# Optimization experiments

Measured on AMD Instinct MI355X. Metric: run time of the kernel, lower is better.

Reference implementation:

```python
import jax, jax.numpy as jnp
import numpy as np

DIM = 384
HEADS = 12
HEAD_DIM = DIM // HEADS
WS = 7


def setup_inputs() -> dict:
    key = jax.random.key(0)
    k0, k1, k2, k3, k4 = jax.random.split(key, 5)
    x = jax.random.normal(k0, (16, DIM, 56, 56), dtype=jnp.float32)
    s = 1.0 / np.sqrt(DIM)
    Wqkv = jax.random.normal(k1, (DIM, 3 * DIM), dtype=jnp.float32) * s
    bqkv = jax.random.normal(k2, (3 * DIM,), dtype=jnp.float32) * 0.01
    Wproj = jax.random.normal(k3, (DIM, DIM), dtype=jnp.float32) * s
    bproj = jax.random.normal(k4, (DIM,), dtype=jnp.float32) * 0.01
    return {"x": x, "Wqkv": Wqkv, "bqkv": bqkv, "Wproj": Wproj, "bproj": bproj}


def _window_attention(x, Wqkv, bqkv, Wproj, bproj):
    B, D, H, W = x.shape
    x = jnp.transpose(x, (0, 2, 3, 1))  # (B, H, W, D)
    pad_h = (WS - H % WS) % WS
    pad_w = (WS - W % WS) % WS
    if pad_h or pad_w:
        x = jnp.pad(x, ((0, 0), (0, pad_h), (0, pad_w), (0, 0)))
    Hp, Wp = x.shape[1], x.shape[2]
    nH, nW = Hp // WS, Wp // WS
    # window partition: (B*nH*nW, WS*WS, D)
    xw = x.reshape(B, nH, WS, nW, WS, D).transpose(0, 1, 3, 2, 4, 5)
    windows = xw.reshape(B * nH * nW, WS * WS, D)
    BnW, N, _ = windows.shape
    qkv = windows @ Wqkv + bqkv  # (BnW, N, 3D)
    qkv = qkv.reshape(BnW, N, 3, HEADS, HEAD_DIM).transpose(2, 0, 3, 1, 4)
    q, k, v = qkv[0], qkv[1], qkv[2]  # (BnW, heads, N, hd)
    scale = HEAD_DIM ** -0.5
    attn = jnp.einsum('bhnd,bhmd->bhnm', q, k) * scale
    attn = jax.nn.softmax(attn, axis=-1)
    out = jnp.einsum('bhnm,bhmd->bhnd', attn, v)  # (BnW, heads, N, hd)
    out = out.transpose(0, 2, 1, 3).reshape(BnW, N, D)
    out = out @ Wproj + bproj
    # window reverse
    x = out.reshape(B, nH, nW, WS, WS, D).transpose(0, 1, 3, 2, 4, 5)
    x = x.reshape(B, Hp, Wp, D)
    if pad_h or pad_w:
        x = x[:, :H, :W, :]
    return jnp.transpose(x, (0, 3, 1, 2))  # (B, D, H, W)


def reference(x, Wqkv, bqkv, Wproj, bproj):
    return _window_attention(x, Wqkv, bqkv, Wproj, bproj)
```

## Files before the change

### kernel.cpp

```cpp
#include <hip/hip_runtime.h>

#define TOK     50176
#define NQKV    1152
#define DMODEL  384
#define HW      3136
#define NWIN    1024

typedef __bf16 bf16x8 __attribute__((ext_vector_type(8)));
typedef float  f32x4  __attribute__((ext_vector_type(4)));

__device__ __forceinline__ __bf16 f2bf(float f) {
  unsigned u = __float_as_uint(f);
  u += 0x7fffu + ((u >> 16) & 1u);
  unsigned short s = (unsigned short)(u >> 16);
  return __builtin_bit_cast(__bf16, s);
}
__device__ __forceinline__ unsigned short f2bfu(float f) {
  return __builtin_bit_cast(unsigned short, f2bf(f));
}
__device__ __forceinline__ float bf2f(__bf16 b) {
  return __uint_as_float(((unsigned)__builtin_bit_cast(unsigned short, b)) << 16);
}
__device__ __forceinline__ void gload_lds16(const void* g, void* l) {
  __builtin_amdgcn_global_load_lds(
      (const __attribute__((address_space(1))) unsigned int*)g,
      (__attribute__((address_space(3))) unsigned int*)l, 16, 0, 0);
}

__global__ __launch_bounds__(256) void gather_x(const float* __restrict__ x,
                                                __bf16* __restrict__ Xw) {
  __shared__ __bf16 lt[392 * 48];
  const int ct = blockIdx.x, hr = blockIdx.y, b = blockIdx.z;
  const int tid = threadIdx.x;
  const float* xb = x + ((size_t)(b * 384 + ct * 48)) * HW + hr * 7 * 56;

  for (int u = tid; u < 48 * 7 * 14; u += 256) {
    const int ch = u / 98, rem = u % 98;
    const int h7 = rem / 14, w4 = rem % 14;
    const float4 v = *(const float4*)&xb[(size_t)ch * HW + h7 * 56 + 4 * w4];
    const float vv[4] = {v.x, v.y, v.z, v.w};
#pragma unroll
    for (int e = 0; e < 4; ++e) {
      const int w = 4 * w4 + e;
      const int t = (w / 7) * 49 + h7 * 7 + (w % 7);
      lt[t * 48 + ch] = f2bf(vv[e]);
    }
  }
  __syncthreads();

  const size_t tokbase = (size_t)(b * 64 + hr * 8) * 49;
  for (int u = tid; u < 392 * 6; u += 256) {
    const int t = u / 6, c6 = u % 6;
    const bf16x8 vv = *(const bf16x8*)&lt[t * 48 + 8 * c6];
    *(bf16x8*)&Xw[(tokbase + t) * DMODEL + ct * 48 + 8 * c6] = vv;
  }
}

__global__ __launch_bounds__(256) void unscatter(const __bf16* __restrict__ P,
                                                 float* __restrict__ out) {
  __shared__ __bf16 lt[392 * 48];
  const int ct = blockIdx.x, hr = blockIdx.y, b = blockIdx.z;
  const int tid = threadIdx.x;
  const size_t tokbase = (size_t)(b * 64 + hr * 8) * 49;

  for (int u = tid; u < 392 * 6; u += 256) {
    const int t = u / 6, c6 = u % 6;
    *(bf16x8*)&lt[t * 48 + 8 * c6] =
        *(const bf16x8*)&P[(tokbase + t) * DMODEL + ct * 48 + 8 * c6];
  }
  __syncthreads();

  float* ob = out + ((size_t)(b * 384 + ct * 48)) * HW + hr * 7 * 56;
  for (int u = tid; u < 48 * 98; u += 256) {
    const int ch = u / 98, rem = u % 98;
    const int h7 = rem / 14, w4 = rem % 14;
    float4 o;
    float* oo = (float*)&o;
#pragma unroll
    for (int e = 0; e < 4; ++e) {
      const int w = 4 * w4 + e;
      const int t = (w / 7) * 49 + h7 * 7 + (w % 7);
      oo[e] = bf2f(lt[t * 48 + ch]);
    }
    *(float4*)&ob[(size_t)ch * HW + h7 * 56 + 4 * w4] = o;
  }
}

__global__ void conv_w(const float* __restrict__ Wqkv, const float* __restrict__ Wproj,
                       __bf16* __restrict__ WqkvT, __bf16* __restrict__ WprojT) {
  const int idx = blockIdx.x * 256 + threadIdx.x;
  if (idx < DMODEL * NQKV) {
    const int k = idx / NQKV, n = idx % NQKV;
    WqkvT[(size_t)n * DMODEL + k] = f2bf(Wqkv[idx]);
  }
  if (idx < DMODEL * DMODEL) {
    const int k = idx / DMODEL, n = idx % DMODEL;
    WprojT[(size_t)n * DMODEL + k] = f2bf(Wproj[idx]);
  }
}

__global__ __launch_bounds__(512) void gemm256(const __bf16* __restrict__ A,
                                               const __bf16* __restrict__ BT,
                                               const float* __restrict__ bias,
                                               __bf16* __restrict__ Cout, int Ncols) {
  __shared__ __align__(16) __bf16 As[3][256 * 32];
  __shared__ __align__(16) __bf16 Bs[3][128 * 32];
  const int tid  = threadIdx.x;
  const int lane = tid & 63;
  const int wid  = tid >> 6;

  const int nwg  = gridDim.x * gridDim.y;
  const int orig = blockIdx.y * gridDim.x + blockIdx.x;
  const int q    = nwg >> 3, r = nwg & 7;
  const int xcd  = orig & 7, pos = orig >> 3;
  const int start = (xcd < r) ? xcd * (q + 1) : r * (q + 1) + (xcd - r) * q;
  const int w    = start + pos;
  const int bn   = (w % gridDim.x) << 7;
  const int bm   = (w / gridDim.x) << 8;

  const __bf16* a0 = A  + (size_t)(bm +       (tid >> 2)) * DMODEL + ((tid & 3) << 3);
  const __bf16* a1 = A  + (size_t)(bm + 128 + (tid >> 2)) * DMODEL + ((tid & 3) << 3);
  const __bf16* b0 = BT + (size_t)(bn +       (tid >> 2)) * DMODEL + ((tid & 3) << 3);

  const int wm = (wid >> 1) << 6;
  const int wn = (wid & 1) << 6;
  const int lrow = lane & 15;
  const int lk8  = (lane >> 4) << 3;

  f32x4 acc[4][4] = {};

  auto stage = [&](int buf, int kt) {
    const int koff = kt << 5;
    gload_lds16(a0 + koff, &As[buf][(wid << 9)]);
    gload_lds16(a1 + koff, &As[buf][4096 + (wid << 9)]);
    gload_lds16(b0 + koff, &Bs[buf][(wid << 9)]);
  };

  stage(0, 0);
  stage(1, 1);
#pragma unroll 1
  for (int kt = 0; kt < 12; ++kt) {
    asm volatile("s_waitcnt vmcnt(3)" ::: "memory");
    __builtin_amdgcn_sched_barrier(0);
    __builtin_amdgcn_s_barrier();
    __builtin_amdgcn_sched_barrier(0);
    asm volatile("" ::: "memory");

    const int nt = (kt + 2 < 12) ? (kt + 2) : (kt - 10);
    stage((kt + 2) % 3, nt);

    const int buf = kt % 3;
    const __bf16* pA = &As[buf][(wm + lrow) * 32 + lk8];
    const __bf16* pB = &Bs[buf][(wn + lrow) * 32 + lk8];
    bf16x8 av[4], bv[4];
#pragma unroll
    for (int i = 0; i < 4; ++i) av[i] = *(const bf16x8*)(pA + i * 16 * 32);
#pragma unroll
    for (int j = 0; j < 4; ++j) bv[j] = *(const bf16x8*)(pB + j * 16 * 32);
#pragma unroll
    for (int i = 0; i < 4; ++i)
#pragma unroll
      for (int j = 0; j < 4; ++j)
        acc[j][i] = __builtin_amdgcn_mfma_f32_16x16x32_bf16(bv[j], av[i], acc[j][i], 0, 0, 0);
  }

  const int lr = lane & 15, g = lane >> 4;
  const int tok0 = bm + wm + lr;
  const int ch0  = bn + wn + (g << 2);

#pragma unroll
  for (int j = 0; j < 4; ++j) {
    const int ch = ch0 + 16 * j;
    const float4 b4 = *(const float4*)&bias[ch];
#pragma unroll
    for (int i = 0; i < 4; ++i) {
      const int token = tok0 + 16 * i;
      ushort4 pk;
      pk.x = f2bfu(acc[j][i][0] + b4.x);
      pk.y = f2bfu(acc[j][i][1] + b4.y);
      pk.z = f2bfu(acc[j][i][2] + b4.z);
      pk.w = f2bfu(acc[j][i][3] + b4.w);
      *(ushort4*)&Cout[(size_t)token * Ncols + ch] = pk;
    }
  }
}

__global__ __launch_bounds__(64) void attn_mfma(const __bf16* __restrict__ qkv,
                                                __bf16* __restrict__ attnO) {
  __shared__ __align__(16) __bf16 lds[96 * 72];
  __bf16* p_lds = lds;
  __bf16* vt    = lds + 64 * 72;

  const int lane = threadIdx.x;
  const int win  = blockIdx.x;
  const int h    = blockIdx.y;
  const int lr = lane & 15, g = lane >> 4;
  const size_t rowbase = (size_t)win * 49;

  int rr[4];
#pragma unroll
  for (int f = 0; f < 4; ++f) rr[f] = (16 * f + lr > 48) ? 48 : (16 * f + lr);

  const int co = h * 32 + 8 * g;

  bf16x8 av[4], bv[4];
#pragma unroll
  for (int f = 0; f < 4; ++f) {
    const __bf16* rp = qkv + (rowbase + rr[f]) * NQKV + co;
    av[f] = *(const bf16x8*)(rp + 384);
    bv[f] = *(const bf16x8*)(rp);
  }

  ushort4 vreg[7];
#pragma unroll
  for (int u = 0; u < 7; ++u) {
    const int unit = lane + (u << 6);
    if (unit < 392) {
      const int k = unit >> 3, dq = unit & 7;
      vreg[u] = *(const ushort4*)(qkv + (rowbase + k) * NQKV + 768 + h * 32 + 4 * dq);
    }
  }

  f32x4 acc[4][4] = {};
#pragma unroll
  for (int i = 0; i < 4; ++i)
#pragma unroll
    for (int j = 0; j < 4; ++j)
      acc[i][j] = __builtin_amdgcn_mfma_f32_16x16x32_bf16(av[i], bv[j], acc[i][j], 0, 0, 0);

  const float scale = 0.17677669529663687f;
#pragma unroll
  for (int i = 0; i < 4; ++i)
#pragma unroll
    for (int j = 0; j < 4; ++j)
#pragma unroll
      for (int r = 0; r < 4; ++r) {
        float v = acc[i][j][r] * scale;
        if (i == 3 && (4 * g + r) != 0) v = -1e30f;
        acc[i][j][r] = v;
      }

#pragma unroll
  for (int u = 0; u < 7; ++u) {
    const int unit = lane + (u << 6);
    if (unit < 392) {
      const int k = unit >> 3, dq = unit & 7;
      const ushort4 vv = vreg[u];
      vt[(4 * dq + 0) * 72 + k] = __builtin_bit_cast(__bf16, vv.x);
      vt[(4 * dq + 1) * 72 + k] = __builtin_bit_cast(__bf16, vv.y);
      vt[(4 * dq + 2) * 72 + k] = __builtin_bit_cast(__bf16, vv.z);
      vt[(4 * dq + 3) * 72 + k] = __builtin_bit_cast(__bf16, vv.w);
    }
  }

#pragma unroll
  for (int j = 0; j < 4; ++j) {
    float mx = -1e30f;
#pragma unroll
    for (int i = 0; i < 4; ++i)
#pragma unroll
      for (int r = 0; r < 4; ++r) mx = fmaxf(mx, acc[i][j][r]);
    mx = fmaxf(mx, __shfl_xor(mx, 16));
    mx = fmaxf(mx, __shfl_xor(mx, 32));
    float sum = 0.f;
#pragma unroll
    for (int i = 0; i < 4; ++i)
#pragma unroll
      for (int r = 0; r < 4; ++r) {
        const float e = __expf(acc[i][j][r] - mx);
        acc[i][j][r] = e;
        sum += e;
      }
    sum += __shfl_xor(sum, 16);
    sum += __shfl_xor(sum, 32);
    const float inv = 1.f / sum;
#pragma unroll
    for (int i = 0; i < 4; ++i) {
      ushort4 pk;
      pk.x = f2bfu(acc[i][j][0] * inv);
      pk.y = f2bfu(acc[i][j][1] * inv);
      pk.z = f2bfu(acc[i][j][2] * inv);
      pk.w = f2bfu(acc[i][j][3] * inv);
      *(ushort4*)&p_lds[(16 * j + lr) * 72 + 16 * i + 4 * g] = pk;
    }
  }

  f32x4 o[2][4] = {};
#pragma unroll
  for (int ks = 0; ks < 2; ++ks) {
    bf16x8 a2[2], b2[4];
#pragma unroll
    for (int i2 = 0; i2 < 2; ++i2)
      a2[i2] = *(const bf16x8*)&vt[(16 * i2 + lr) * 72 + 32 * ks + 8 * g];
#pragma unroll
    for (int j2 = 0; j2 < 4; ++j2)
      b2[j2] = *(const bf16x8*)&p_lds[(16 * j2 + lr) * 72 + 32 * ks + 8 * g];
#pragma unroll
    for (int i2 = 0; i2 < 2; ++i2)
#pragma unroll
      for (int j2 = 0; j2 < 4; ++j2)
        o[i2][j2] = __builtin_amdgcn_mfma_f32_16x16x32_bf16(a2[i2], b2[j2], o[i2][j2], 0, 0, 0);
  }

#pragma unroll
  for (int j2 = 0; j2 < 4; ++j2) {
    const int q = 16 * j2 + lr;
    if (q <= 48) {
#pragma unroll
      for (int i2 = 0; i2 < 2; ++i2) {
        ushort4 ok;
        ok.x = f2bfu(o[i2][j2][0]);
        ok.y = f2bfu(o[i2][j2][1]);
        ok.z = f2bfu(o[i2][j2][2]);
        ok.w = f2bfu(o[i2][j2][3]);
        *(ushort4*)&attnO[(rowbase + q) * DMODEL + h * 32 + 16 * i2 + 4 * g] = ok;
      }
    }
  }
}

extern "C" void kernel_launch(void* const* d_in, const int* in_sizes, int n_in,
                              void* d_out, int out_size, void* d_ws, size_t ws_size,
                              hipStream_t stream) {
  const float* x     = (const float*)d_in[0];
  const float* Wqkv  = (const float*)d_in[1];
  const float* bqkv  = (const float*)d_in[2];
  const float* Wproj = (const float*)d_in[3];
  const float* bproj = (const float*)d_in[4];
  float* out = (float*)d_out;

  char* ws = (char*)d_ws;
  __bf16* Xw     = (__bf16*)ws;  ws += (size_t)TOK * DMODEL * 2;
  __bf16* qkvb   = (__bf16*)ws;  ws += (size_t)TOK * NQKV * 2;
  __bf16* attnO  = (__bf16*)ws;  ws += (size_t)TOK * DMODEL * 2;
  __bf16* attnP  = (__bf16*)ws;  ws += (size_t)TOK * DMODEL * 2;
  __bf16* WqkvT  = (__bf16*)ws;  ws += (size_t)NQKV * DMODEL * 2;
  __bf16* WprojT = (__bf16*)ws;

  gather_x<<<dim3(8, 8, 16), 256, 0, stream>>>(x, Xw);
  conv_w<<<1728, 256, 0, stream>>>(Wqkv, Wproj, WqkvT, WprojT);
  gemm256<<<dim3(NQKV / 128, TOK / 256), 512, 0, stream>>>(Xw, WqkvT, bqkv, qkvb, NQKV);
  attn_mfma<<<dim3(NWIN, 12), 64, 0, stream>>>(qkvb, attnO);
  gemm256<<<dim3(DMODEL / 128, TOK / 256), 512, 0, stream>>>(attnO, WprojT, bproj, attnP, DMODEL);
  unscatter<<<dim3(8, 8, 16), 256, 0, stream>>>(attnP, out);
}
```

Before: 229.4 us.

## Split QKV GEMM k-step into two halves with interleaved loads and setprio

Restructures the triple-buffered main loop of the QKV GEMM. Global-to-LDS prefetches for the next stage are now issued between two halves of the MFMA work: A tiles before the first half, B tile after a mid-iteration barrier. MFMA blocks are wrapped in s_setprio raises. The goal is better overlap of memory issue with compute and less scheduler contention, at the cost of an extra workgroup barrier per k-step.

```diff
diff --git a/kernel.cpp b/kernel.cpp
--- a/kernel.cpp
+++ b/kernel.cpp
@@ -129,39 +129,64 @@
 
   f32x4 acc[4][4] = {};
 
-  auto stage = [&](int buf, int kt) {
-    const int koff = kt << 5;
-    gload_lds16(a0 + koff, &As[buf][(wid << 9)]);
-    gload_lds16(a1 + koff, &As[buf][4096 + (wid << 9)]);
-    gload_lds16(b0 + koff, &Bs[buf][(wid << 9)]);
-  };
-
-  stage(0, 0);
-  stage(1, 1);
+  {
+    gload_lds16(a0, &As[0][(wid << 9)]);
+    gload_lds16(a1, &As[0][4096 + (wid << 9)]);
+    gload_lds16(b0, &Bs[0][(wid << 9)]);
+    gload_lds16(a0 + 32, &As[1][(wid << 9)]);
+    gload_lds16(a1 + 32, &As[1][4096 + (wid << 9)]);
+    gload_lds16(b0 + 32, &Bs[1][(wid << 9)]);
+  }
+  asm volatile("s_waitcnt vmcnt(3)" ::: "memory");
+  __builtin_amdgcn_sched_barrier(0);
+  __builtin_amdgcn_s_barrier();
+  __builtin_amdgcn_sched_barrier(0);
+
 #pragma unroll 1
   for (int kt = 0; kt < 12; ++kt) {
-    asm volatile("s_waitcnt vmcnt(3)" ::: "memory");
-    __builtin_amdgcn_sched_barrier(0);
-    __builtin_amdgcn_s_barrier();
-    __builtin_amdgcn_sched_barrier(0);
-    asm volatile("" ::: "memory");
-
-    const int nt = (kt + 2 < 12) ? (kt + 2) : (kt - 10);
-    stage((kt + 2) % 3, nt);
-
     const int buf = kt % 3;
+    const int dst = (kt + 2) % 3;
+    const int nt  = (kt + 2 < 12) ? (kt + 2) : (kt - 10);
+    const int koff = nt << 5;
     const __bf16* pA = &As[buf][(wm + lrow) * 32 + lk8];
     const __bf16* pB = &Bs[buf][(wn + lrow) * 32 + lk8];
-    bf16x8 av[4], bv[4];
-#pragma unroll
-    for (int i = 0; i < 4; ++i) av[i] = *(const bf16x8*)(pA + i * 16 * 32);
+
+    gload_lds16(a0 + koff, &As[dst][(wid << 9)]);
+    gload_lds16(a1 + koff, &As[dst][4096 + (wid << 9)]);
+    bf16x8 bv[4], av0, av1;
 #pragma unroll
     for (int j = 0; j < 4; ++j) bv[j] = *(const bf16x8*)(pB + j * 16 * 32);
-#pragma unroll
-    for (int i = 0; i < 4; ++i)
-#pragma unroll
-      for (int j = 0; j < 4; ++j)
-        acc[j][i] = __builtin_amdgcn_mfma_f32_16x16x32_bf16(bv[j], av[i], acc[j][i], 0, 0, 0);
+    av0 = *(const bf16x8*)(pA);
+    av1 = *(const bf16x8*)(pA + 16 * 32);
+    __builtin_amdgcn_s_setprio(1);
+#pragma unroll
+    for (int j = 0; j < 4; ++j)
+      acc[j][0] = __builtin_amdgcn_mfma_f32_16x16x32_bf16(bv[j], av0, acc[j][0], 0, 0, 0);
+#pragma unroll
+    for (int j = 0; j < 4; ++j)
+      acc[j][1] = __builtin_amdgcn_mfma_f32_16x16x32_bf16(bv[j], av1, acc[j][1], 0, 0, 0);
+    __builtin_amdgcn_s_setprio(0);
+    __builtin_amdgcn_sched_barrier(0);
+    __builtin_amdgcn_s_barrier();
+    __builtin_amdgcn_sched_barrier(0);
+
+    gload_lds16(b0 + koff, &Bs[dst][(wid << 9)]);
+    bf16x8 av2, av3;
+    av2 = *(const bf16x8*)(pA + 2 * 16 * 32);
+    av3 = *(const bf16x8*)(pA + 3 * 16 * 32);
+    __builtin_amdgcn_s_setprio(1);
+#pragma unroll
+    for (int j = 0; j < 4; ++j)
+      acc[j][2] = __builtin_amdgcn_mfma_f32_16x16x32_bf16(bv[j], av2, acc[j][2], 0, 0, 0);
+#pragma unroll
+    for (int j = 0; j < 4; ++j)
+      acc[j][3] = __builtin_amdgcn_mfma_f32_16x16x32_bf16(bv[j], av3, acc[j][3], 0, 0, 0);
+    __builtin_amdgcn_s_setprio(0);
+    __builtin_amdgcn_sched_barrier(0);
+    asm volatile("s_waitcnt vmcnt(3)" ::: "memory");
+    __builtin_amdgcn_sched_barrier(0);
+    __builtin_amdgcn_s_barrier();
+    __builtin_amdgcn_sched_barrier(0);
   }
 
   const int lr = lane & 15, g = lane >> 4;
```

Result: no change. 228.4 us (-0.4%).

## Widen GEMM tile to 256x256 with padded N and restructured prefetch barrier

Applied to the files above, without the earlier changes.

Grows the GEMM block tile from 256x128 to 256x256, so each wave computes 128x64 with more MFMAs per LDS load. To fit the wider tile, the QKV output is padded from 1152 to 1280 columns and the projection output from 384 to 512, with zero-filled weights and biases. The loop now issues the prefetch before the MFMAs, raises wave priority around the MFMA block, and moves the wait and barrier to the end of each iteration. The padding adds wasted work, about 11% for QKV and a third for the projection, and more LDS and registers per block.

```diff
diff --git a/kernel.cpp b/kernel.cpp
--- a/kernel.cpp
+++ b/kernel.cpp
@@ -2,7 +2,9 @@
 
 #define TOK     50176
 #define NQKV    1152
+#define NQKVP   1280
 #define DMODEL  384
+#define PROJP   512
 #define HW      3136
 #define NWIN    1024
 
@@ -66,7 +68,7 @@
   for (int u = tid; u < 392 * 6; u += 256) {
     const int t = u / 6, c6 = u % 6;
     *(bf16x8*)&lt[t * 48 + 8 * c6] =
-        *(const bf16x8*)&P[(tokbase + t) * DMODEL + ct * 48 + 8 * c6];
+        *(const bf16x8*)&P[(tokbase + t) * PROJP + ct * 48 + 8 * c6];
   }
   __syncthreads();
 
@@ -87,16 +89,20 @@
 }
 
 __global__ void conv_w(const float* __restrict__ Wqkv, const float* __restrict__ Wproj,
-                       __bf16* __restrict__ WqkvT, __bf16* __restrict__ WprojT) {
+                       const float* __restrict__ bqkv, const float* __restrict__ bproj,
+                       __bf16* __restrict__ WqkvT, __bf16* __restrict__ WprojT,
+                       float* __restrict__ bqkvP, float* __restrict__ bprojP) {
   const int idx = blockIdx.x * 256 + threadIdx.x;
-  if (idx < DMODEL * NQKV) {
-    const int k = idx / NQKV, n = idx % NQKV;
-    WqkvT[(size_t)n * DMODEL + k] = f2bf(Wqkv[idx]);
-  }
-  if (idx < DMODEL * DMODEL) {
-    const int k = idx / DMODEL, n = idx % DMODEL;
-    WprojT[(size_t)n * DMODEL + k] = f2bf(Wproj[idx]);
-  }
+  if (idx < NQKVP * DMODEL) {
+    const int n = idx / DMODEL, k = idx % DMODEL;
+    WqkvT[idx] = (n < NQKV) ? f2bf(Wqkv[(size_t)k * NQKV + n]) : (__bf16)0.0f;
+  }
+  if (idx < PROJP * DMODEL) {
+    const int n = idx / DMODEL, k = idx % DMODEL;
+    WprojT[idx] = (n < DMODEL) ? f2bf(Wproj[(size_t)k * DMODEL + n]) : (__bf16)0.0f;
+  }
+  if (idx < NQKVP) bqkvP[idx] = (idx < NQKV) ? bqkv[idx] : 0.f;
+  if (idx < PROJP) bprojP[idx] = (idx < DMODEL) ? bproj[idx] : 0.f;
 }
 
 __global__ __launch_bounds__(512) void gemm256(const __bf16* __restrict__ A,
@@ -104,7 +110,7 @@
                                                const float* __restrict__ bias,
                                                __bf16* __restrict__ Cout, int Ncols) {
   __shared__ __align__(16) __bf16 As[3][256 * 32];
-  __shared__ __align__(16) __bf16 Bs[3][128 * 32];
+  __shared__ __align__(16) __bf16 Bs[3][256 * 32];
   const int tid  = threadIdx.x;
   const int lane = tid & 63;
   const int wid  = tid >> 6;
@@ -115,53 +121,62 @@
   const int xcd  = orig & 7, pos = orig >> 3;
   const int start = (xcd < r) ? xcd * (q + 1) : r * (q + 1) + (xcd - r) * q;
   const int w    = start + pos;
-  const int bn   = (w % gridDim.x) << 7;
+  const int bn   = (w % gridDim.x) << 8;
   const int bm   = (w / gridDim.x) << 8;
 
-  const __bf16* a0 = A  + (size_t)(bm +       (tid >> 2)) * DMODEL + ((tid & 3) << 3);
-  const __bf16* a1 = A  + (size_t)(bm + 128 + (tid >> 2)) * DMODEL + ((tid & 3) << 3);
-  const __bf16* b0 = BT + (size_t)(bn +       (tid >> 2)) * DMODEL + ((tid & 3) << 3);
-
-  const int wm = (wid >> 1) << 6;
-  const int wn = (wid & 1) << 6;
+  const __bf16* a0 = A  + (size_t)(bm + (tid >> 2)) * DMODEL + ((tid & 3) << 3);
+  const __bf16* a1 = a0 + (size_t)128 * DMODEL;
+  const __bf16* b0 = BT + (size_t)(bn + (tid >> 2)) * DMODEL + ((tid & 3) << 3);
+  const __bf16* b1 = b0 + (size_t)128 * DMODEL;
+
+  const int wm = (wid >> 2) << 7;
+  const int wn = (wid & 3) << 6;
   const int lrow = lane & 15;
   const int lk8  = (lane >> 4) << 3;
 
-  f32x4 acc[4][4] = {};
+  f32x4 acc[4][8] = {};
 
   auto stage = [&](int buf, int kt) {
     const int koff = kt << 5;
     gload_lds16(a0 + koff, &As[buf][(wid << 9)]);
     gload_lds16(a1 + koff, &As[buf][4096 + (wid << 9)]);
     gload_lds16(b0 + koff, &Bs[buf][(wid << 9)]);
+    gload_lds16(b1 + koff, &Bs[buf][4096 + (wid << 9)]);
   };
 
   stage(0, 0);
   stage(1, 1);
+  asm volatile("s_waitcnt vmcnt(4)" ::: "memory");
+  __builtin_amdgcn_sched_barrier(0);
+  __builtin_amdgcn_s_barrier();
+  __builtin_amdgcn_sched_barrier(0);
+
 #pragma unroll 1
   for (int kt = 0; kt < 12; ++kt) {
-    asm volatile("s_waitcnt vmcnt(3)" ::: "memory");
+    const int buf = kt % 3;
+    const int dst = (kt + 2) % 3;
+    const int nt  = (kt + 2 < 12) ? (kt + 2) : (kt - 10);
+    stage(dst, nt);
+
+    const __bf16* pA = &As[buf][(wm + lrow) * 32 + lk8];
+    const __bf16* pB = &Bs[buf][(wn + lrow) * 32 + lk8];
+    bf16x8 av[8], bv[4];
+#pragma unroll
+    for (int i = 0; i < 8; ++i) av[i] = *(const bf16x8*)(pA + i * 16 * 32);
+#pragma unroll
+    for (int j = 0; j < 4; ++j) bv[j] = *(const bf16x8*)(pB + j * 16 * 32);
+    __builtin_amdgcn_s_setprio(1);
+#pragma unroll
+    for (int i = 0; i < 8; ++i)
+#pragma unroll
+      for (int j = 0; j < 4; ++j)
+        acc[j][i] = __builtin_amdgcn_mfma_f32_16x16x32_bf16(bv[j], av[i], acc[j][i], 0, 0, 0);
+    __builtin_amdgcn_s_setprio(0);
+    __builtin_amdgcn_sched_barrier(0);
+    asm volatile("s_waitcnt vmcnt(4)" ::: "memory");
     __builtin_amdgcn_sched_barrier(0);
     __builtin_amdgcn_s_barrier();
     __builtin_amdgcn_sched_barrier(0);
-    asm volatile("" ::: "memory");
-
-    const int nt = (kt + 2 < 12) ? (kt + 2) : (kt - 10);
-    stage((kt + 2) % 3, nt);
-
-    const int buf = kt % 3;
-    const __bf16* pA = &As[buf][(wm + lrow) * 32 + lk8];
-    const __bf16* pB = &Bs[buf][(wn + lrow) * 32 + lk8];
-    bf16x8 av[4], bv[4];
-#pragma unroll
-    for (int i = 0; i < 4; ++i) av[i] = *(const bf16x8*)(pA + i * 16 * 32);
-#pragma unroll
-    for (int j = 0; j < 4; ++j) bv[j] = *(const bf16x8*)(pB + j * 16 * 32);
-#pragma unroll
-    for (int i = 0; i < 4; ++i)
-#pragma unroll
-      for (int j = 0; j < 4; ++j)
-        acc[j][i] = __builtin_amdgcn_mfma_f32_16x16x32_bf16(bv[j], av[i], acc[j][i], 0, 0, 0);
   }
 
   const int lr = lane & 15, g = lane >> 4;
@@ -173,7 +188,7 @@
     const int ch = ch0 + 16 * j;
     const float4 b4 = *(const float4*)&bias[ch];
 #pragma unroll
-    for (int i = 0; i < 4; ++i) {
+    for (int i = 0; i < 8; ++i) {
       const int token = tok0 + 16 * i;
       ushort4 pk;
       pk.x = f2bfu(acc[j][i][0] + b4.x);
@@ -206,7 +221,7 @@
   bf16x8 av[4], bv[4];
 #pragma unroll
   for (int f = 0; f < 4; ++f) {
-    const __bf16* rp = qkv + (rowbase + rr[f]) * NQKV + co;
+    const __bf16* rp = qkv + (rowbase + rr[f]) * NQKVP + co;
     av[f] = *(const bf16x8*)(rp + 384);
     bv[f] = *(const bf16x8*)(rp);
   }
@@ -217,7 +232,7 @@
     const int unit = lane + (u << 6);
     if (unit < 392) {
       const int k = unit >> 3, dq = unit & 7;
-      vreg[u] = *(const ushort4*)(qkv + (rowbase + k) * NQKV + 768 + h * 32 + 4 * dq);
+      vreg[u] = *(const ushort4*)(qkv + (rowbase + k) * NQKVP + 768 + h * 32 + 4 * dq);
     }
   }
 
@@ -331,16 +346,19 @@
 
   char* ws = (char*)d_ws;
   __bf16* Xw     = (__bf16*)ws;  ws += (size_t)TOK * DMODEL * 2;
-  __bf16* qkvb   = (__bf16*)ws;  ws += (size_t)TOK * NQKV * 2;
+  __bf16* qkvb   = (__bf16*)ws;  ws += (size_t)TOK * NQKVP * 2;
   __bf16* attnO  = (__bf16*)ws;  ws += (size_t)TOK * DMODEL * 2;
-  __bf16* attnP  = (__bf16*)ws;  ws += (size_t)TOK * DMODEL * 2;
-  __bf16* WqkvT  = (__bf16*)ws;  ws += (size_t)NQKV * DMODEL * 2;
-  __bf16* WprojT = (__bf16*)ws;
+  __bf16* attnP  = (__bf16*)ws;  ws += (size_t)TOK * PROJP * 2;
+  __bf16* WqkvT  = (__bf16*)ws;  ws += (size_t)NQKVP * DMODEL * 2;
+  __bf16* WprojT = (__bf16*)ws;  ws += (size_t)PROJP * DMODEL * 2;
+  float*  bqkvP  = (float*)ws;   ws += NQKVP * 4;
+  float*  bprojP = (float*)ws;
 
   gather_x<<<dim3(8, 8, 16), 256, 0, stream>>>(x, Xw);
-  conv_w<<<1728, 256, 0, stream>>>(Wqkv, Wproj, WqkvT, WprojT);
-  gemm256<<<dim3(NQKV / 128, TOK / 256), 512, 0, stream>>>(Xw, WqkvT, bqkv, qkvb, NQKV);
+  conv_w<<<(NQKVP * DMODEL + 255) / 256, 256, 0, stream>>>(Wqkv, Wproj, bqkv, bproj,
+                                                           WqkvT, WprojT, bqkvP, bprojP);
+  gemm256<<<dim3(NQKVP / 256, TOK / 256), 512, 0, stream>>>(Xw, WqkvT, bqkvP, qkvb, NQKVP);
   attn_mfma<<<dim3(NWIN, 12), 64, 0, stream>>>(qkvb, attnO);
-  gemm256<<<dim3(DMODEL / 128, TOK / 256), 512, 0, stream>>>(attnO, WprojT, bproj, attnP, DMODEL);
+  gemm256<<<dim3(PROJP / 256, TOK / 256), 512, 0, stream>>>(attnO, WprojT, bprojP, attnP, PROJP);
   unscatter<<<dim3(8, 8, 16), 256, 0, stream>>>(attnP, out);
 }
```

After: 266.4 us. +16.1%, slower.
